# Performance work log

Hardware: AMD Instinct MI355X
Metric: run time of the kernel (lower is better)

The kernel has to match this reference:

```python
import jax, jax.numpy as jnp
from jax import lax
import numpy as np

EPS = 1e-5  # BatchNorm eps


def setup_inputs() -> dict:
    key = jax.random.key(0)
    ks = jax.random.split(key, 4)
    T, B, C = 256, 128, 1024
    L, H, NCLS = 6, 1024, 1000
    x = jax.random.normal(ks[0], (T, B, C), dtype=jnp.float32)
    W = jax.random.normal(ks[1], (L, C, H), dtype=jnp.float32) * (1.0 / np.sqrt(C))
    b = jnp.zeros((L, H), dtype=jnp.float32)
    gamma = jnp.ones((L, H), dtype=jnp.float32)
    beta = jnp.zeros((L, H), dtype=jnp.float32)
    u = jax.random.uniform(ks[2], (L, H), dtype=jnp.float32)  # recurrent weights in (0, U_bound~1)
    Wc = jax.random.normal(ks[3], (H, NCLS), dtype=jnp.float32) * (1.0 / np.sqrt(H))
    bc = jnp.zeros((NCLS,), dtype=jnp.float32)
    return {"x": x, "W": W, "b": b, "gamma": gamma, "beta": beta, "u": u, "Wc": Wc, "bc": bc}


def _layer(h, Wl, bl, gl, betal, ul):
    # per-timestep dense projection: [T,B,Cin] @ [Cin,H]
    z = jnp.einsum('tbi,ih->tbh', h, Wl) + bl
    # BN over (time, batch) per channel (bn_before, training-mode batch stats)
    mean = jnp.mean(z, axis=(0, 1))
    var = jnp.var(z, axis=(0, 1))
    z = (z - mean) * (gl / jnp.sqrt(var + EPS)) + betal
    # IndRNN diagonal recurrence: h_t = relu(z_t + u * h_{t-1}), h_0 = 0
    T, B, H = z.shape
    def step(hprev, zt):
        hnew = jax.nn.relu(zt + ul * hprev)
        return hnew, hnew
    _, hs = lax.scan(step, jnp.zeros((B, H), dtype=z.dtype), z)
    return hs


def reference(x, W, b, gamma, beta, u, Wc, bc):
    h = x
    for l in range(W.shape[0]):
        h = _layer(h, W[l], b[l], gamma[l], beta[l], u[l])
    # classifier on last timestep
    return h[-1] @ Wc + bc
```

## Files before the change

### kernel.cpp

```cpp
#include <hip/hip_runtime.h>
#include <hip/hip_bf16.h>

#define T_DIM 256
#define B_DIM 128
#define C_DIM 1024
#define H_DIM 1024
#define L_DIM 6
#define NC_DIM 1000
#define M_DIM (T_DIM * B_DIM)
#define BH_DIM (B_DIM * H_DIM)

typedef __attribute__((ext_vector_type(8))) short bf16x8;
typedef __attribute__((ext_vector_type(4))) float f32x4;

__device__ __forceinline__ float bf2f(unsigned short u) {
  union { unsigned int i; float f; } v; v.i = ((unsigned int)u) << 16; return v.f;
}
__device__ __forceinline__ unsigned short f2bf(float f) {
  union { float f; unsigned int i; } v; v.f = f;
  unsigned int r = v.i + 0x7fffu + ((v.i >> 16) & 1u);
  return (unsigned short)(r >> 16);
}
__device__ __forceinline__ unsigned int pack2bf(float lo, float hi) {
  __hip_bfloat162 b2 = __float22bfloat162_rn(float2{lo, hi});
  union { __hip_bfloat162 b; unsigned int u; } cv; cv.b = b2; return cv.u;
}

__device__ __forceinline__ void gload_lds16(const void* g, void* l) {
  __builtin_amdgcn_global_load_lds(
      (const __attribute__((address_space(1))) unsigned int*)g,
      (__attribute__((address_space(3))) unsigned int*)l, 16, 0, 0);
}

__global__ __launch_bounds__(256) void f32_to_bf16_kernel(
    const float* __restrict__ in, unsigned short* __restrict__ out, int n4) {
  int stride = gridDim.x * blockDim.x;
  for (int i = blockIdx.x * blockDim.x + threadIdx.x; i < n4; i += stride) {
    float4 v = ((const float4*)in)[i];
    unsigned int lo = pack2bf(v.x, v.y);
    unsigned int hi = pack2bf(v.z, v.w);
    uint2 o; o.x = lo; o.y = hi;
    ((uint2*)out)[i] = o;
  }
}

__global__ __launch_bounds__(256) void wtrans_kernel(
    const float* __restrict__ W, unsigned short* __restrict__ Wt) {
  __shared__ float tile[32][33];
  int l = blockIdx.z;
  const float* Wl = W + (size_t)l * C_DIM * H_DIM;
  unsigned short* Wtl = Wt + (size_t)l * C_DIM * H_DIM;
  int h0 = blockIdx.x * 32, c0 = blockIdx.y * 32;
  int tx = threadIdx.x, ty = threadIdx.y;
#pragma unroll
  for (int i = 0; i < 32; i += 8)
    tile[ty + i][tx] = Wl[(size_t)(c0 + ty + i) * H_DIM + h0 + tx];
  __syncthreads();
#pragma unroll
  for (int i = 0; i < 32; i += 8)
    Wtl[(size_t)(h0 + ty + i) * C_DIM + c0 + tx] = f2bf(tile[tx][ty + i]);
}

#define NT 32

__global__ __launch_bounds__(512, 2) void gemm_kernel(
    const unsigned short* __restrict__ A, const unsigned short* __restrict__ Bt,
    unsigned short* __restrict__ Z, float* __restrict__ psum, float* __restrict__ psqs) {
  extern __shared__ char lds[];
  int bid = blockIdx.x;
  int swz = (bid & 7) * 32 + (bid >> 3);
  int tm0 = (swz >> 2) * 2;
  int tn = swz & 3;
  int tid = threadIdx.x;
  int wv = tid >> 6, ln = tid & 63;
  int wm = wv >> 2, wn = wv & 3;

  const char* Ap0 = (const char*)A + (size_t)tm0 * 256 * 2048;
  const char* Ap1 = Ap0 + (size_t)256 * 2048;
  const char* Bpanel = (const char*)Bt + (size_t)tn * 256 * 2048;

  int p0 = wv * 1024 + ln * 16;
  int l0 = p0 ^ (((p0 >> 7) & 3) << 4);
  size_t ro0 = (size_t)(p0 >> 6) * 2048 + (l0 & 63);
  size_t ro1 = (size_t)(128 + (p0 >> 6)) * 2048 + (l0 & 63);
  int sdst = wv * 1024;

  auto stage = [&](const char* Ap, int t) {
    char* base = lds + ((t & 3) * 32768);
    int kb = t * 64;
    gload_lds16(Ap + ro0 + kb, base + sdst);
    gload_lds16(Ap + ro1 + kb, base + 8192 + sdst);
    gload_lds16(Bpanel + ro0 + kb, base + 16384 + sdst);
    gload_lds16(Bpanel + ro1 + kb, base + 16384 + 8192 + sdst);
  };

  int frow = ln & 15;
  int fchunk = ((ln >> 4) ^ (frow >> 1)) & 3;
  int floff = frow * 64 + (fchunk << 4);

  f32x4 acc[8][4];

  bf16x8 bX[4], aP[4], aQ[4];
  auto readB_to = [&](int t, bf16x8* d) {
    const char* Bb = lds + ((t & 3) * 32768) + 16384 + wn * 4096;
#pragma unroll
    for (int n = 0; n < 4; ++n) d[n] = *(const bf16x8*)(Bb + n * 1024 + floff);
  };
  auto readA_to = [&](int t, int mq, bf16x8* d) {
    const char* Ab = lds + ((t & 3) * 32768) + wm * 8192 + mq * 4096;
#pragma unroll
    for (int i = 0; i < 4; ++i) d[i] = *(const bf16x8*)(Ab + i * 1024 + floff);
  };

  auto kloop = [&](const char* Ap) {
    f32x4 zero = {0.f, 0.f, 0.f, 0.f};
#pragma unroll
    for (int m = 0; m < 8; ++m)
#pragma unroll
      for (int n = 0; n < 4; ++n) acc[m][n] = zero;
    readB_to(0, bX); readA_to(0, 0, aP);
    for (int t = 0; t < NT; ++t) {
      readA_to(t, 1, aQ);
      if (t <= NT - 4) stage(Ap, t + 3);
      __builtin_amdgcn_s_setprio(1);
#pragma unroll
      for (int i = 0; i < 4; ++i)
#pragma unroll
        for (int n = 0; n < 4; ++n)
          acc[i][n] = __builtin_amdgcn_mfma_f32_16x16x32_bf16(aP[i], bX[n], acc[i][n], 0, 0, 0);
      __builtin_amdgcn_s_setprio(0);
      __builtin_amdgcn_s_setprio(1);
#pragma unroll
      for (int i = 0; i < 4; ++i)
#pragma unroll
        for (int n = 0; n < 4; ++n)
          acc[4 + i][n] = __builtin_amdgcn_mfma_f32_16x16x32_bf16(aQ[i], bX[n], acc[4 + i][n], 0, 0, 0);
      __builtin_amdgcn_s_setprio(0);
      if (t < NT - 1) {
        readB_to(t + 1, bX); readA_to(t + 1, 0, aP);
        if (t <= NT - 4) { asm volatile("s_waitcnt vmcnt(4)" ::: "memory"); }
        else             { asm volatile("s_waitcnt vmcnt(0)" ::: "memory"); }
        __builtin_amdgcn_s_barrier();
      }
    }
  };

  float* red = (float*)(lds + 3 * 32768);
  auto epilogue = [&](int tm) {
    float s[4], q[4];
#pragma unroll
    for (int n = 0; n < 4; ++n) {
      float sv = 0.f, qv = 0.f;
#pragma unroll
      for (int m = 0; m < 8; ++m)
#pragma unroll
        for (int r = 0; r < 4; ++r) {
          float v = acc[m][n][r];
          sv += v; qv += v * v;
        }
      s[n] = sv; q[n] = qv;
    }
#pragma unroll
    for (int n = 0; n < 4; ++n) {
      s[n] += __shfl_xor(s[n], 16); s[n] += __shfl_xor(s[n], 32);
      q[n] += __shfl_xor(q[n], 16); q[n] += __shfl_xor(q[n], 32);
    }
    if (ln < 16) {
#pragma unroll
      for (int n = 0; n < 4; ++n) {
        red[wm * 256 + wn * 64 + n * 16 + ln] = s[n];
        red[512 + wm * 256 + wn * 64 + n * 16 + ln] = q[n];
      }
    }
    __syncthreads();
    if (tid < 256) {
      psum[(size_t)tm * H_DIM + tn * 256 + tid] = red[tid] + red[256 + tid];
    } else {
      int c = tid - 256;
      psqs[(size_t)tm * H_DIM + tn * 256 + c] = red[512 + c] + red[768 + c];
    }
    __syncthreads();
    int r0 = tm * 256 + wm * 128 + ((ln >> 4) << 2);
    int c0 = tn * 256 + wn * 64 + (ln & 15);
#pragma unroll
    for (int m = 0; m < 8; ++m)
#pragma unroll
      for (int n = 0; n < 4; ++n) {
        unsigned short* zp = Z + (size_t)(r0 + m * 16) * H_DIM + c0 + n * 16;
#pragma unroll
        for (int r = 0; r < 4; ++r) zp[(size_t)r * H_DIM] = f2bf(acc[m][n][r]);
      }
  };

  stage(Ap0, 0); stage(Ap0, 1); stage(Ap0, 2);
  asm volatile("s_waitcnt vmcnt(4)" ::: "memory");
  __builtin_amdgcn_s_barrier();
  kloop(Ap0);
  __builtin_amdgcn_s_barrier();
  stage(Ap1, 0); stage(Ap1, 1); stage(Ap1, 2);
  epilogue(tm0);
  asm volatile("s_waitcnt vmcnt(4)" ::: "memory");
  __builtin_amdgcn_s_barrier();
  kloop(Ap1);
  __builtin_amdgcn_s_barrier();
  epilogue(tm0 + 1);
}

__global__ __launch_bounds__(256) void bn_finalize_kernel(
    const float* __restrict__ psum, const float* __restrict__ psqs,
    const float* __restrict__ gamma, const float* __restrict__ beta,
    float* __restrict__ ss) {
  int c = blockIdx.x * blockDim.x + threadIdx.x;
  float s = 0.f, q = 0.f;
#pragma unroll 8
  for (int i = 0; i < 128; ++i) {
    s += psum[(size_t)i * H_DIM + c];
    q += psqs[(size_t)i * H_DIM + c];
  }
  const float invN = 1.0f / (float)M_DIM;
  float mean = s * invN;
  float var = q * invN - mean * mean;
  float sc = gamma[c] * rsqrtf(var + 1e-5f);
  ss[c] = sc;
  ss[H_DIM + c] = beta[c] - mean * sc;
}

__global__ __launch_bounds__(256) void bn_recur_kernel(
    const unsigned short* __restrict__ Z, const float* __restrict__ ss,
    const float* __restrict__ u, unsigned short* __restrict__ Hout) {
  int i2 = blockIdx.x * 256 + threadIdx.x;
  int h0 = (i2 & (H_DIM / 2 - 1)) * 2;
  float sc0 = ss[h0], sc1 = ss[h0 + 1];
  float sh0 = ss[H_DIM + h0], sh1 = ss[H_DIM + h0 + 1];
  float u0 = u[h0], u1 = u[h0 + 1];
  float hv0 = 0.f, hv1 = 0.f;

  const size_t ST = BH_DIM / 2;
  const unsigned int* Zt = (const unsigned int*)Z + i2;
  unsigned int* Ht = (unsigned int*)Hout + i2;

  unsigned int za[32], zb[32], ho[32];
#pragma unroll
  for (int j = 0; j < 32; ++j) za[j] = Zt[(size_t)j * ST];

#pragma unroll
  for (int blk = 0; blk < 4; ++blk) {
    int tA = blk * 64;
#pragma unroll
    for (int j = 0; j < 32; ++j) zb[j] = Zt[(size_t)(tA + 32 + j) * ST];
#pragma unroll
    for (int j = 0; j < 32; ++j) {
      unsigned int zz = za[j];
      float z0 = fmaf(bf2f((unsigned short)(zz & 0xffffu)), sc0, sh0);
      float z1 = fmaf(bf2f((unsigned short)(zz >> 16)), sc1, sh1);
      hv0 = fmaxf(fmaf(u0, hv0, z0), 0.f);
      hv1 = fmaxf(fmaf(u1, hv1, z1), 0.f);
      ho[j] = pack2bf(hv0, hv1);
    }
#pragma unroll
    for (int j = 0; j < 32; ++j) Ht[(size_t)(tA + j) * ST] = ho[j];
    if (blk < 3) {
#pragma unroll
      for (int j = 0; j < 32; ++j) za[j] = Zt[(size_t)(tA + 64 + j) * ST];
    }
#pragma unroll
    for (int j = 0; j < 32; ++j) {
      unsigned int zz = zb[j];
      float z0 = fmaf(bf2f((unsigned short)(zz & 0xffffu)), sc0, sh0);
      float z1 = fmaf(bf2f((unsigned short)(zz >> 16)), sc1, sh1);
      hv0 = fmaxf(fmaf(u0, hv0, z0), 0.f);
      hv1 = fmaxf(fmaf(u1, hv1, z1), 0.f);
      ho[j] = pack2bf(hv0, hv1);
    }
#pragma unroll
    for (int j = 0; j < 32; ++j) Ht[(size_t)(tA + 32 + j) * ST] = ho[j];
  }
}

__global__ __launch_bounds__(256) void classifier_kernel(
    const unsigned short* __restrict__ hlast, const float* __restrict__ Wc,
    const float* __restrict__ bc, float* __restrict__ out) {
  __shared__ float hs[H_DIM];
  int b = blockIdx.y;
  int n = blockIdx.x * 256 + threadIdx.x;
  for (int k = threadIdx.x; k < H_DIM; k += 256)
    hs[k] = bf2f(hlast[(size_t)b * H_DIM + k]);
  __syncthreads();
  if (n < NC_DIM) {
    float acc = bc[n];
#pragma unroll 8
    for (int k = 0; k < H_DIM; ++k)
      acc = fmaf(hs[k], Wc[(size_t)k * NC_DIM + n], acc);
    out[(size_t)b * NC_DIM + n] = acc;
  }
}

extern "C" void kernel_launch(void* const* d_in, const int* in_sizes, int n_in,
                              void* d_out, int out_size, void* d_ws, size_t ws_size,
                              hipStream_t stream) {
  const float* x     = (const float*)d_in[0];
  const float* W     = (const float*)d_in[1];
  const float* gamma = (const float*)d_in[3];
  const float* beta  = (const float*)d_in[4];
  const float* u     = (const float*)d_in[5];
  const float* Wc    = (const float*)d_in[6];
  const float* bc    = (const float*)d_in[7];
  float* out = (float*)d_out;

  const size_t CH = (size_t)C_DIM * H_DIM;
  const size_t MH = (size_t)M_DIM * H_DIM;
  char* p = (char*)d_ws;
  unsigned short* Wt = (unsigned short*)p; p += L_DIM * CH * sizeof(unsigned short);
  unsigned short* Ha = (unsigned short*)p; p += MH * sizeof(unsigned short);
  unsigned short* Hb = (unsigned short*)p; p += MH * sizeof(unsigned short);
  unsigned short* Z  = (unsigned short*)p; p += MH * sizeof(unsigned short);
  float* psum = (float*)p; p += 128 * H_DIM * sizeof(float);
  float* psqs = (float*)p; p += 128 * H_DIM * sizeof(float);
  float* ss   = (float*)p; p += 2 * H_DIM * sizeof(float);

  f32_to_bf16_kernel<<<2048, 256, 0, stream>>>(x, Ha, (int)(MH / 4));
  wtrans_kernel<<<dim3(H_DIM / 32, C_DIM / 32, L_DIM), dim3(32, 8), 0, stream>>>(W, Wt);

  unsigned short* cur = Ha;
  unsigned short* nxt = Hb;
  for (int l = 0; l < L_DIM; ++l) {
    gemm_kernel<<<256, 512, 131072, stream>>>(cur, Wt + (size_t)l * CH, Z, psum, psqs);
    bn_finalize_kernel<<<4, 256, 0, stream>>>(psum, psqs, gamma + (size_t)l * H_DIM,
                                              beta + (size_t)l * H_DIM, ss);
    bn_recur_kernel<<<BH_DIM / 512, 256, 0, stream>>>(Z, ss, u + (size_t)l * H_DIM, nxt);
    unsigned short* tmp = cur; cur = nxt; nxt = tmp;
  }
  classifier_kernel<<<dim3(4, B_DIM), 256, 0, stream>>>(
      cur + (size_t)(T_DIM - 1) * BH_DIM, Wc, bc, out);
}
```

Before: 769.7 us.

## Skip unused last-layer stores, parallelize BN finalize, batch classifier rows

In the final layer the recurrence kernel now writes only the last timestep, because that is the only one the classifier reads. This removes a full T*B*H bf16 store. The BN finalize kernel now spreads the 128-partial reduction over 32 blocks with a shared-memory combine, instead of 4 blocks each looping serially. The classifier processes 8 batch rows per block so each Wc load is reused 8 times. The cost is more shared memory and registers per block and a per-store branch in the recurrence loop.

```diff
diff --git a/kernel.cpp b/kernel.cpp
--- a/kernel.cpp
+++ b/kernel.cpp
@@ -37,9 +37,7 @@
   int stride = gridDim.x * blockDim.x;
   for (int i = blockIdx.x * blockDim.x + threadIdx.x; i < n4; i += stride) {
     float4 v = ((const float4*)in)[i];
-    unsigned int lo = pack2bf(v.x, v.y);
-    unsigned int hi = pack2bf(v.z, v.w);
-    uint2 o; o.x = lo; o.y = hi;
+    uint2 o; o.x = pack2bf(v.x, v.y); o.y = pack2bf(v.z, v.w);
     ((uint2*)out)[i] = o;
   }
 }
@@ -210,24 +208,36 @@
     const float* __restrict__ psum, const float* __restrict__ psqs,
     const float* __restrict__ gamma, const float* __restrict__ beta,
     float* __restrict__ ss) {
-  int c = blockIdx.x * blockDim.x + threadIdx.x;
+  __shared__ float sred[2][8][32];
+  int c0 = blockIdx.x * 32;
+  int cl = threadIdx.x & 31, jg = threadIdx.x >> 5;
   float s = 0.f, q = 0.f;
-#pragma unroll 8
-  for (int i = 0; i < 128; ++i) {
-    s += psum[(size_t)i * H_DIM + c];
-    q += psqs[(size_t)i * H_DIM + c];
-  }
-  const float invN = 1.0f / (float)M_DIM;
-  float mean = s * invN;
-  float var = q * invN - mean * mean;
-  float sc = gamma[c] * rsqrtf(var + 1e-5f);
-  ss[c] = sc;
-  ss[H_DIM + c] = beta[c] - mean * sc;
+#pragma unroll
+  for (int j = 0; j < 16; ++j) {
+    size_t row = (size_t)(jg * 16 + j) * H_DIM + c0 + cl;
+    s += psum[row];
+    q += psqs[row];
+  }
+  sred[0][jg][cl] = s;
+  sred[1][jg][cl] = q;
+  __syncthreads();
+  if (threadIdx.x < 32) {
+    int c = threadIdx.x;
+    float ts = 0.f, tq = 0.f;
+#pragma unroll
+    for (int g = 0; g < 8; ++g) { ts += sred[0][g][c]; tq += sred[1][g][c]; }
+    const float invN = 1.0f / (float)M_DIM;
+    float mean = ts * invN;
+    float var = tq * invN - mean * mean;
+    float sc = gamma[c0 + c] * rsqrtf(var + 1e-5f);
+    ss[c0 + c] = sc;
+    ss[H_DIM + c0 + c] = beta[c0 + c] - mean * sc;
+  }
 }
 
 __global__ __launch_bounds__(256) void bn_recur_kernel(
     const unsigned short* __restrict__ Z, const float* __restrict__ ss,
-    const float* __restrict__ u, unsigned short* __restrict__ Hout) {
+    const float* __restrict__ u, unsigned short* __restrict__ Hout, int full) {
   int i2 = blockIdx.x * 256 + threadIdx.x;
   int h0 = (i2 & (H_DIM / 2 - 1)) * 2;
   float sc0 = ss[h0], sc1 = ss[h0 + 1];
@@ -258,7 +268,8 @@
       ho[j] = pack2bf(hv0, hv1);
     }
 #pragma unroll
-    for (int j = 0; j < 32; ++j) Ht[(size_t)(tA + j) * ST] = ho[j];
+    for (int j = 0; j < 32; ++j)
+      if (full || (tA + j) == T_DIM - 1) Ht[(size_t)(tA + j) * ST] = ho[j];
     if (blk < 3) {
 #pragma unroll
       for (int j = 0; j < 32; ++j) za[j] = Zt[(size_t)(tA + 64 + j) * ST];
@@ -273,25 +284,35 @@
       ho[j] = pack2bf(hv0, hv1);
     }
 #pragma unroll
-    for (int j = 0; j < 32; ++j) Ht[(size_t)(tA + 32 + j) * ST] = ho[j];
+    for (int j = 0; j < 32; ++j)
+      if (full || (tA + 32 + j) == T_DIM - 1) Ht[(size_t)(tA + 32 + j) * ST] = ho[j];
   }
 }
 
 __global__ __launch_bounds__(256) void classifier_kernel(
     const unsigned short* __restrict__ hlast, const float* __restrict__ Wc,
     const float* __restrict__ bc, float* __restrict__ out) {
-  __shared__ float hs[H_DIM];
-  int b = blockIdx.y;
+  __shared__ float hs[8][H_DIM];
+  int b0 = blockIdx.y * 8;
   int n = blockIdx.x * 256 + threadIdx.x;
-  for (int k = threadIdx.x; k < H_DIM; k += 256)
-    hs[k] = bf2f(hlast[(size_t)b * H_DIM + k]);
+#pragma unroll
+  for (int r = 0; r < 8; ++r)
+    for (int k = threadIdx.x; k < H_DIM; k += 256)
+      hs[r][k] = bf2f(hlast[(size_t)(b0 + r) * H_DIM + k]);
   __syncthreads();
   if (n < NC_DIM) {
-    float acc = bc[n];
-#pragma unroll 8
-    for (int k = 0; k < H_DIM; ++k)
-      acc = fmaf(hs[k], Wc[(size_t)k * NC_DIM + n], acc);
-    out[(size_t)b * NC_DIM + n] = acc;
+    float acc[8];
+#pragma unroll
+    for (int r = 0; r < 8; ++r) acc[r] = bc[n];
+#pragma unroll 4
+    for (int k = 0; k < H_DIM; ++k) {
+      float w = Wc[(size_t)k * NC_DIM + n];
+#pragma unroll
+      for (int r = 0; r < 8; ++r) acc[r] = fmaf(hs[r][k], w, acc[r]);
+    }
+#pragma unroll
+    for (int r = 0; r < 8; ++r)
+      out[(size_t)(b0 + r) * NC_DIM + n] = acc[r];
   }
 }
 
@@ -325,11 +346,12 @@
   unsigned short* nxt = Hb;
   for (int l = 0; l < L_DIM; ++l) {
     gemm_kernel<<<256, 512, 131072, stream>>>(cur, Wt + (size_t)l * CH, Z, psum, psqs);
-    bn_finalize_kernel<<<4, 256, 0, stream>>>(psum, psqs, gamma + (size_t)l * H_DIM,
-                                              beta + (size_t)l * H_DIM, ss);
-    bn_recur_kernel<<<BH_DIM / 512, 256, 0, stream>>>(Z, ss, u + (size_t)l * H_DIM, nxt);
+    bn_finalize_kernel<<<32, 256, 0, stream>>>(psum, psqs, gamma + (size_t)l * H_DIM,
+                                               beta + (size_t)l * H_DIM, ss);
+    bn_recur_kernel<<<BH_DIM / 512, 256, 0, stream>>>(Z, ss, u + (size_t)l * H_DIM, nxt,
+                                                      (l < L_DIM - 1) ? 1 : 0);
     unsigned short* tmp = cur; cur = nxt; nxt = tmp;
   }
-  classifier_kernel<<<dim3(4, B_DIM), 256, 0, stream>>>(
+  classifier_kernel<<<dim3(4, B_DIM / 8), 256, 0, stream>>>(
       cur + (size_t)(T_DIM - 1) * BH_DIM, Wc, bc, out);
 }
```

Measured after the change: 752.5 us. 2.2% less time.
